# Performance work log

Measured on AMD Instinct MI355X. Metric: run time of the kernel, lower is better.

The kernel has to match this reference:

```python
import jax, jax.numpy as jnp
import numpy as np

N, E, F, H, L, G, O = 100000, 1600000, 128, 128, 4, 512, 10
BN_EPS = 1e-5


def setup_inputs() -> dict:
    key = jax.random.key(0)
    ks = jax.random.split(key, 12)
    x = jax.random.normal(ks[0], (N, F), dtype=jnp.float32)
    edge_index = jax.random.randint(ks[1], (2, E), 0, N, dtype=jnp.int32)
    batch = jnp.sort(jax.random.randint(ks[2], (N,), 0, G, dtype=jnp.int32))
    s = 1.0 / np.sqrt(H)
    # 4 GIN layers, input_dim == hidden_dim so params stack uniformly
    W1s = jax.random.uniform(ks[3], (L, F, H), jnp.float32, -s, s)
    b1s = jnp.zeros((L, H), jnp.float32)
    W2s = jax.random.uniform(ks[4], (L, H, H), jnp.float32, -s, s)
    b2s = jnp.zeros((L, H), jnp.float32)
    eps = jnp.zeros((L,), jnp.float32)  # learnable eps, init 0
    gammas = jnp.ones((L, H), jnp.float32)
    betas = jnp.zeros((L, H), jnp.float32)
    Din = F + L * H  # concatenated graph embedding dim
    so = 1.0 / np.sqrt(Din)
    Wout = jax.random.uniform(ks[5], (Din, O), jnp.float32, -so, so)
    bout = jnp.zeros((O,), jnp.float32)
    return {"x": x, "edge_index": edge_index, "batch": batch,
            "W1s": W1s, "b1s": b1s, "W2s": W2s, "b2s": b2s, "eps": eps,
            "gammas": gammas, "betas": betas, "Wout": Wout, "bout": bout}


def reference(x, edge_index, batch, W1s, b1s, W2s, b2s, eps, gammas, betas, Wout, bout):
    src, dst = edge_index[0], edge_index[1]
    n = x.shape[0]
    pooled = [jax.ops.segment_sum(x, batch, num_segments=G)]  # [G, F]
    h = x
    for l in range(W1s.shape[0]):
        # GINConv: MLP((1+eps)*h + sum_{j in N(i)} h_j)
        agg = jax.ops.segment_sum(h[src], dst, num_segments=n)  # [N, H]
        z = (1.0 + eps[l]) * h + agg
        z = jax.nn.relu(z @ W1s[l] + b1s[l]) @ W2s[l] + b2s[l]
        # BatchNorm1d (batch statistics, biased variance) + ReLU; dropout=identity (eval)
        mu = z.mean(axis=0)
        var = z.var(axis=0)
        z = (z - mu) * jax.lax.rsqrt(var + BN_EPS) * gammas[l] + betas[l]
        h = jax.nn.relu(z)
        pooled.append(jax.ops.segment_sum(h, batch, num_segments=G))  # [G, H]
    emb = jnp.concatenate(pooled, axis=1)  # [G, F + L*H]
    return emb @ Wout + bout  # [G, O]
```

## Files before the change

### kernel.cpp

```cpp
#include <hip/hip_runtime.h>
#include <hip/hip_bf16.h>

typedef __attribute__((ext_vector_type(8))) __bf16 bf16x8;
typedef __attribute__((ext_vector_type(4))) float f32x4;
typedef unsigned short u16;
typedef unsigned int u32;

constexpr int Nn = 100000;
constexpr int Ee = 1600000;
constexpr int Hd = 128;
constexpr int Ll = 4;
constexpr int Gg = 512;
constexpr int Oo = 10;
constexpr int Din = Hd + Ll * Hd;
constexpr int PSPLIT = 4;
constexpr int NBLK = (Nn + 127) / 128;
constexpr int AGG_BLKS = 8192;

constexpr int NB = 256;
constexpr int NPB = 392;
constexpr int BCAP = 8192;
constexpr int BATCH = 8192;
constexpr int NBATCH = (Ee + BATCH - 1) / BATCH;
constexpr int XCVT_BLKS = Nn * Hd / 8 / 256;
constexpr int WPREP_BLKS = Ll * 2 * Hd * Hd / 256;
constexpr float BN_EPS = 1e-5f;

__device__ __forceinline__ int swzb(int row, int bc) {
  return (row << 8) + (bc ^ ((row & 7) << 4));
}

__device__ __forceinline__ u16 f2bf(float f) {
  __hip_bfloat16 b = __float2bfloat16(f);
  u16 u;
  __builtin_memcpy(&u, &b, 2);
  return u;
}

__device__ __forceinline__ float bf2f(u32 u) { return __uint_as_float(u << 16); }

__device__ __forceinline__ int lower_bound_dev(const int* a, int n, int key) {
  int lo = 0, hi = n;
  while (lo < hi) { int mid = (lo + hi) >> 1; if (a[mid] < key) lo = mid + 1; else hi = mid; }
  return lo;
}

__device__ __forceinline__ void bn_param(const float* __restrict__ stats,
                                         const float* __restrict__ gammas,
                                         const float* __restrict__ betas,
                                         int prevL, int f, float& sc, float& sh) {
  const float invn = 1.0f / (float)Nn;
  float mu = stats[f] * invn;
  float var = stats[128 + f] * invn - mu * mu;
  sc = gammas[prevL * Hd + f] * rsqrtf(var + BN_EPS);
  sh = betas[prevL * Hd + f] - mu * sc;
}

__device__ __forceinline__ void gload_lds16(const void* g, void* l) {
  __builtin_amdgcn_global_load_lds((const __attribute__((address_space(1))) unsigned int*)g,
                                   (__attribute__((address_space(3))) unsigned int*)l, 16, 0, 0);
}

__global__ __launch_bounds__(256) void prep_kernel(const float* __restrict__ x, __hip_bfloat16* __restrict__ xb,
                                                   const float* __restrict__ W1s, const float* __restrict__ W2s,
                                                   __hip_bfloat16* __restrict__ wt,
                                                   int* __restrict__ gptr,
                                                   const int* __restrict__ batch, int* __restrict__ gb,
                                                   float* __restrict__ out, float* __restrict__ statsAll) {
  int b = blockIdx.x;
  int tid = threadIdx.x;
  if (b < XCVT_BLKS) {
    int i = b * 256 + tid;
    f32x4 v0 = *(const f32x4*)(x + (size_t)i * 8);
    f32x4 v1 = *(const f32x4*)(x + (size_t)i * 8 + 4);
    uint4 o;
    o.x = (u32)f2bf(v0[0]) | ((u32)f2bf(v0[1]) << 16);
    o.y = (u32)f2bf(v0[2]) | ((u32)f2bf(v0[3]) << 16);
    o.z = (u32)f2bf(v1[0]) | ((u32)f2bf(v1[1]) << 16);
    o.w = (u32)f2bf(v1[2]) | ((u32)f2bf(v1[3]) << 16);
    *(uint4*)((u16*)xb + (size_t)i * 8) = o;
  } else if (b < XCVT_BLKS + WPREP_BLKS) {
    int idx = (b - XCVT_BLKS) * 256 + tid;
    int l = idx >> 15;
    int w = (idx >> 14) & 1;
    int nn = (idx >> 7) & 127;
    int k = idx & 127;
    const float* W = w ? W2s : W1s;
    wt[idx] = __float2bfloat16(W[l * Hd * Hd + k * Hd + nn]);
  } else if (b == XCVT_BLKS + WPREP_BLKS) {
    gptr[tid] = tid * BCAP;
    for (int g = tid; g <= Gg; g += 256)
      gb[g] = (g == Gg) ? Nn : lower_bound_dev(batch, Nn, g);
  } else {
    for (int i = tid; i < Gg * Oo; i += 256) out[i] = 0.f;
    for (int i = tid; i < Ll * 256; i += 256) statsAll[i] = 0.f;
  }
}

__global__ __launch_bounds__(256) void binA_kernel(const int* __restrict__ src, const int* __restrict__ dst,
                                                   int* __restrict__ gptr, u32* __restrict__ buckets) {
  __shared__ int hist[NB];
  __shared__ int lbase[NB];
  __shared__ int lpos[NB];
  __shared__ int gbaseS[NB];
  __shared__ int scanT[NB];
  __shared__ u32 reorder[BATCH];
  const int tid = threadIdx.x;
  const int e0 = blockIdx.x * BATCH;
  const int n = min(BATCH, Ee - e0);

  hist[tid] = 0;
  __syncthreads();
  for (int k = tid; k < n; k += 256) {
    int d = dst[e0 + k];
    atomicAdd(&hist[d / NPB], 1);
  }
  __syncthreads();
  int v = hist[tid];
  scanT[tid] = v;
  __syncthreads();
  for (int off = 1; off < NB; off <<= 1) {
    int x = (tid >= off) ? scanT[tid - off] : 0;
    __syncthreads();
    scanT[tid] += x;
    __syncthreads();
  }
  lbase[tid] = scanT[tid] - v;
  lpos[tid] = 0;
  __syncthreads();
  for (int k = tid; k < n; k += 256) {
    int d = dst[e0 + k];
    int s = src[e0 + k];
    int b = d / NPB;
    int dlo = d - b * NPB;
    int p = lbase[b] + atomicAdd(&lpos[b], 1);
    reorder[p] = ((u32)dlo << 17) | (u32)s;
  }
  __syncthreads();
  if (hist[tid] > 0) gbaseS[tid] = atomicAdd(&gptr[tid], hist[tid]);
  __syncthreads();
  for (int p = tid; p < n; p += 256) {
    int lo = 0, hi = NB - 1;
    while (lo < hi) { int mid = (lo + hi + 1) >> 1; if (lbase[mid] <= p) lo = mid; else hi = mid - 1; }
    buckets[gbaseS[lo] + (p - lbase[lo])] = reorder[p];
  }
}

__global__ __launch_bounds__(512) void place_kernel(const u32* __restrict__ buckets,
                                                    const int* __restrict__ gptr,
                                                    int* __restrict__ indptr, int* __restrict__ adj) {
  __shared__ int cntS[NB];
  __shared__ int scanS[NB];
  __shared__ int ncnt[512];
  __shared__ int nofs[NPB];
  __shared__ int lcur[NPB];
  const int tid = threadIdx.x;
  const int b = blockIdx.x;

  if (tid < NB) {
    int c = gptr[tid] - tid * BCAP;
    cntS[tid] = c;
    scanS[tid] = c;
  }
  __syncthreads();
  for (int off = 1; off < NB; off <<= 1) {
    int x = 0;
    if (tid < NB && tid >= off) x = scanS[tid - off];
    __syncthreads();
    if (tid < NB) scanS[tid] += x;
    __syncthreads();
  }
  const int cnt = cntS[b];
  const int adjbase = scanS[b] - cnt;
  const int ebase = b * BCAP;
  const int node0 = b * NPB;
  const int nnodes = min(NPB, Nn - node0);

  ncnt[tid] = 0;
  if (tid < NPB) lcur[tid] = 0;
  __syncthreads();
  for (int k = tid; k < cnt; k += 512) atomicAdd(&ncnt[buckets[ebase + k] >> 17], 1);
  __syncthreads();
  int v = ncnt[tid];
  for (int off = 1; off < 512; off <<= 1) {
    int x = (tid >= off) ? ncnt[tid - off] : 0;
    __syncthreads();
    ncnt[tid] += x;
    __syncthreads();
  }
  if (tid < NPB) nofs[tid] = ncnt[tid] - v;
  __syncthreads();
  if (tid < nnodes) indptr[node0 + tid] = adjbase + nofs[tid];
  if (tid == 0 && b == 0) indptr[Nn] = Ee;
  for (int k = tid; k < cnt; k += 512) {
    u32 u = buckets[ebase + k];
    int dlo = u >> 17;
    int s = (int)(u & 0x1FFFFu);
    int p = atomicAdd(&lcur[dlo], 1);
    adj[adjbase + nofs[dlo] + p] = s;
  }
}

__global__ __launch_bounds__(256) void agg_kernel(const __hip_bfloat16* __restrict__ zprev,
                                                  const int* __restrict__ indptr,
                                                  const int* __restrict__ adj,
                                                  const float* __restrict__ stats,
                                                  const float* __restrict__ gammas,
                                                  const float* __restrict__ betas,
                                                  const float* __restrict__ epsp,
                                                  int layer, float negLim,
                                                  __hip_bfloat16* __restrict__ t) {
  const int gwave = blockIdx.x * 4 + (threadIdx.x >> 6);
  const int nwaves = AGG_BLKS * 4;
  const int lane = threadIdx.x & 63;
  const int cb = lane * 2;
  const u16* zp = (const u16*)zprev;
  float sc0 = 1.f, sh0 = 0.f, sc1 = 1.f, sh1 = 0.f;
  if (layer > 0) {
    bn_param(stats, gammas, betas, layer - 1, cb, sc0, sh0);
    bn_param(stats, gammas, betas, layer - 1, cb + 1, sc1, sh1);
  }
  const float eps1 = 1.0f + epsp[layer];

  for (int node = gwave; node < Nn; node += nwaves) {
    int s = __builtin_amdgcn_readfirstlane(indptr[node]);
    int e = __builtin_amdgcn_readfirstlane(indptr[node + 1]);
    float a0 = 0.f, a1 = 0.f;
    int p = s;
    while (p + 16 <= e) {
      u32 v[16];
      #pragma unroll
      for (int j = 0; j < 16; ++j) v[j] = *(const u32*)(zp + (size_t)adj[p + j] * Hd + cb);
      #pragma unroll
      for (int j = 0; j < 16; ++j) {
        a0 += fmaxf(fmaf(bf2f(v[j] & 0xffffu), sc0, sh0), negLim);
        a1 += fmaxf(fmaf(bf2f(v[j] >> 16), sc1, sh1), negLim);
      }
      p += 16;
    }
    if (p + 8 <= e) {
      u32 v[8];
      #pragma unroll
      for (int j = 0; j < 8; ++j) v[j] = *(const u32*)(zp + (size_t)adj[p + j] * Hd + cb);
      #pragma unroll
      for (int j = 0; j < 8; ++j) {
        a0 += fmaxf(fmaf(bf2f(v[j] & 0xffffu), sc0, sh0), negLim);
        a1 += fmaxf(fmaf(bf2f(v[j] >> 16), sc1, sh1), negLim);
      }
      p += 8;
    }
    if (p + 4 <= e) {
      u32 v[4];
      #pragma unroll
      for (int j = 0; j < 4; ++j) v[j] = *(const u32*)(zp + (size_t)adj[p + j] * Hd + cb);
      #pragma unroll
      for (int j = 0; j < 4; ++j) {
        a0 += fmaxf(fmaf(bf2f(v[j] & 0xffffu), sc0, sh0), negLim);
        a1 += fmaxf(fmaf(bf2f(v[j] >> 16), sc1, sh1), negLim);
      }
      p += 4;
    }
    for (; p < e; ++p) {
      u32 v0 = *(const u32*)(zp + (size_t)adj[p] * Hd + cb);
      a0 += fmaxf(fmaf(bf2f(v0 & 0xffffu), sc0, sh0), negLim);
      a1 += fmaxf(fmaf(bf2f(v0 >> 16), sc1, sh1), negLim);
    }
    u32 sv = *(const u32*)(zp + (size_t)node * Hd + cb);
    float s0 = fmaxf(fmaf(bf2f(sv & 0xffffu), sc0, sh0), negLim);
    float s1 = fmaxf(fmaf(bf2f(sv >> 16), sc1, sh1), negLim);
    float t0 = eps1 * s0 + a0;
    float t1 = eps1 * s1 + a1;
    *(u32*)((u16*)t + (size_t)node * Hd + cb) = (u32)f2bf(t0) | ((u32)f2bf(t1) << 16);
  }
}

__global__ __launch_bounds__(256) void mlp_kernel(const __hip_bfloat16* __restrict__ t,
                                                  const __hip_bfloat16* __restrict__ w1t,
                                                  const __hip_bfloat16* __restrict__ w2t,
                                                  const float* __restrict__ b1,
                                                  const float* __restrict__ b2,
                                                  __hip_bfloat16* __restrict__ z,
                                                  float* __restrict__ stats) {
  __shared__ __align__(16) unsigned char sA[32 * 1024];
  __shared__ __align__(16) unsigned char sW[32 * 1024];
  const int tid = threadIdx.x;
  const int m0 = blockIdx.x * 128;
  const int lane = tid & 63;
  const int wave = tid >> 6;

  #pragma unroll
  for (int blk = 0; blk < 8; ++blk) {
    const int chunk = wave * 512 + blk * 64 + lane;
    const int row = chunk >> 4, pos = chunk & 15;
    const int spos = pos ^ (row & 7);
    void* ldst = sA + (size_t)(wave * 512 + blk * 64) * 16;
    void* ldstW = sW + (size_t)(wave * 512 + blk * 64) * 16;
    gload_lds16((const unsigned char*)w1t + row * 256 + spos * 16, ldstW);
    gload_lds16((const unsigned char*)t + (size_t)(m0 + row) * 256 + spos * 16, ldst);
  }
  __syncthreads();

  const int lrow = lane & 15;
  const int lkb = (lane >> 4) << 4;
  const int wm = wave * 32;
  const int crow = (lane >> 4) << 2;

  f32x4 acc[2][8];
  #pragma unroll
  for (int a = 0; a < 2; ++a) {
    #pragma unroll
    for (int b = 0; b < 8; ++b) acc[a][b] = (f32x4){0.f, 0.f, 0.f, 0.f};
  }

  #pragma unroll
  for (int kk = 0; kk < 4; ++kk) {
    const int kb2 = kk * 64 + lkb;
    bf16x8 a0 = *(const bf16x8*)(sA + swzb(wm + lrow, kb2));
    bf16x8 a1 = *(const bf16x8*)(sA + swzb(wm + 16 + lrow, kb2));
    #pragma unroll
    for (int nf = 0; nf < 8; ++nf) {
      bf16x8 bfr = *(const bf16x8*)(sW + swzb(nf * 16 + lrow, kb2));
      acc[0][nf] = __builtin_amdgcn_mfma_f32_16x16x32_bf16(a0, bfr, acc[0][nf], 0, 0, 0);
      acc[1][nf] = __builtin_amdgcn_mfma_f32_16x16x32_bf16(a1, bfr, acc[1][nf], 0, 0, 0);
    }
  }
  __syncthreads();

  #pragma unroll
  for (int blk = 0; blk < 8; ++blk) {
    const int chunk = wave * 512 + blk * 64 + lane;
    const int row = chunk >> 4, pos = chunk & 15;
    const int spos = pos ^ (row & 7);
    gload_lds16((const unsigned char*)w2t + row * 256 + spos * 16,
                sW + (size_t)(wave * 512 + blk * 64) * 16);
  }
  #pragma unroll
  for (int nf = 0; nf < 8; ++nf) {
    const int col = nf * 16 + lrow;
    const float bb = b1[col];
    #pragma unroll
    for (int mf = 0; mf < 2; ++mf) {
      #pragma unroll
      for (int j = 0; j < 4; ++j) {
        float v = acc[mf][nf][j] + bb;
        v = v > 0.f ? v : 0.f;
        int row = wm + mf * 16 + crow + j;
        *(u16*)(sA + swzb(row, col * 2)) = f2bf(v);
      }
    }
  }
  __syncthreads();

  f32x4 acc2[2][8];
  #pragma unroll
  for (int a = 0; a < 2; ++a) {
    #pragma unroll
    for (int b = 0; b < 8; ++b) acc2[a][b] = (f32x4){0.f, 0.f, 0.f, 0.f};
  }
  #pragma unroll
  for (int kk = 0; kk < 4; ++kk) {
    const int kb2 = kk * 64 + lkb;
    bf16x8 a0 = *(const bf16x8*)(sA + swzb(wm + lrow, kb2));
    bf16x8 a1 = *(const bf16x8*)(sA + swzb(wm + 16 + lrow, kb2));
    #pragma unroll
    for (int nf = 0; nf < 8; ++nf) {
      bf16x8 bfr = *(const bf16x8*)(sW + swzb(nf * 16 + lrow, kb2));
      acc2[0][nf] = __builtin_amdgcn_mfma_f32_16x16x32_bf16(a0, bfr, acc2[0][nf], 0, 0, 0);
      acc2[1][nf] = __builtin_amdgcn_mfma_f32_16x16x32_bf16(a1, bfr, acc2[1][nf], 0, 0, 0);
    }
  }
  __syncthreads();

  float* sred = (float*)sA;
  float* qred = (float*)(sA + 2048);
  u16* zp = (u16*)z;
  #pragma unroll
  for (int nf = 0; nf < 8; ++nf) {
    const int col = nf * 16 + lrow;
    const float bb = b2[col];
    float s = 0.f, q = 0.f;
    #pragma unroll
    for (int mf = 0; mf < 2; ++mf) {
      #pragma unroll
      for (int j = 0; j < 4; ++j) {
        int grow = m0 + wm + mf * 16 + crow + j;
        if (grow < Nn) {
          float v = acc2[mf][nf][j] + bb;
          zp[(size_t)grow * Hd + col] = f2bf(v);
          s += v; q += v * v;
        }
      }
    }
    s += __shfl_xor(s, 16, 64); s += __shfl_xor(s, 32, 64);
    q += __shfl_xor(q, 16, 64); q += __shfl_xor(q, 32, 64);
    if (lane < 16) { sred[wave * 128 + col] = s; qred[wave * 128 + col] = q; }
  }
  __syncthreads();
  if (tid < 128) {
    float a = sred[tid] + sred[128 + tid] + sred[256 + tid] + sred[384 + tid];
    atomicAdd(&stats[tid], a);
  } else {
    int c = tid - 128;
    float a = qred[c] + qred[128 + c] + qred[256 + c] + qred[384 + c];
    atomicAdd(&stats[128 + c], a);
  }
}

__global__ __launch_bounds__(128) void pool_out_kernel(const __hip_bfloat16* __restrict__ xb,
                                                       const __hip_bfloat16* __restrict__ z0,
                                                       const __hip_bfloat16* __restrict__ z1,
                                                       const __hip_bfloat16* __restrict__ z2,
                                                       const __hip_bfloat16* __restrict__ z3,
                                                       const float* __restrict__ statsAll,
                                                       const float* __restrict__ gammas,
                                                       const float* __restrict__ betas,
                                                       const int* __restrict__ gb,
                                                       const float* __restrict__ Wout,
                                                       const float* __restrict__ bout,
                                                       float* __restrict__ out) {
  const int b = blockIdx.x;
  const int s = b / (Gg * PSPLIT);
  const int rem = b % (Gg * PSPLIT);
  const int g = rem / PSPLIT, sp = rem % PSPLIT;
  const __hip_bfloat16* zsrc = (s == 0) ? xb : (s == 1) ? z0 : (s == 2) ? z1 : (s == 3) ? z2 : z3;
  const float negLim = (s == 0) ? -3.4e38f : 0.f;
  const int colOff = s * Hd;
  const int c2 = (threadIdx.x & 63) * 2;
  const int rh = threadIdx.x >> 6;
  const int lane = threadIdx.x & 63;
  float sc0 = 1.f, sh0 = 0.f, sc1 = 1.f, sh1 = 0.f;
  if (s > 0) {
    bn_param(statsAll + (size_t)(s - 1) * 256, gammas, betas, s - 1, c2, sc0, sh0);
    bn_param(statsAll + (size_t)(s - 1) * 256, gammas, betas, s - 1, c2 + 1, sc1, sh1);
  }
  const int lo = gb[g], hi = gb[g + 1];
  const int len = hi - lo;
  const int chunk = (len + PSPLIT - 1) / PSPLIT;
  const int rs = lo + sp * chunk;
  const int re = min(rs + chunk, hi);
  const u16* zp = (const u16*)zsrc;
  float a0 = 0.f, a1 = 0.f, b0 = 0.f, b1v = 0.f, d0 = 0.f, d1 = 0.f, e0 = 0.f, e1 = 0.f;
  int i = rs + rh;
  for (; i + 6 < re; i += 8) {
    u32 v0 = *(const u32*)(zp + (size_t)i * Hd + c2);
    u32 v1 = *(const u32*)(zp + (size_t)(i + 2) * Hd + c2);
    u32 v2 = *(const u32*)(zp + (size_t)(i + 4) * Hd + c2);
    u32 v3 = *(const u32*)(zp + (size_t)(i + 6) * Hd + c2);
    a0 += fmaxf(fmaf(bf2f(v0 & 0xffffu), sc0, sh0), negLim);
    a1 += fmaxf(fmaf(bf2f(v0 >> 16), sc1, sh1), negLim);
    b0 += fmaxf(fmaf(bf2f(v1 & 0xffffu), sc0, sh0), negLim);
    b1v += fmaxf(fmaf(bf2f(v1 >> 16), sc1, sh1), negLim);
    d0 += fmaxf(fmaf(bf2f(v2 & 0xffffu), sc0, sh0), negLim);
    d1 += fmaxf(fmaf(bf2f(v2 >> 16), sc1, sh1), negLim);
    e0 += fmaxf(fmaf(bf2f(v3 & 0xffffu), sc0, sh0), negLim);
    e1 += fmaxf(fmaf(bf2f(v3 >> 16), sc1, sh1), negLim);
  }
  for (; i < re; i += 2) {
    u32 v = *(const u32*)(zp + (size_t)i * Hd + c2);
    a0 += fmaxf(fmaf(bf2f(v & 0xffffu), sc0, sh0), negLim);
    a1 += fmaxf(fmaf(bf2f(v >> 16), sc1, sh1), negLim);
  }
  a0 += b0 + d0 + e0;
  a1 += b1v + d1 + e1;

  float po[Oo];
  #pragma unroll
  for (int o = 0; o < Oo; ++o)
    po[o] = a0 * Wout[(colOff + c2) * Oo + o] + a1 * Wout[(colOff + c2 + 1) * Oo + o];
  #pragma unroll
  for (int off = 32; off > 0; off >>= 1) {
    #pragma unroll
    for (int o = 0; o < Oo; ++o) po[o] += __shfl_down(po[o], off, 64);
  }
  __shared__ float red[2][Oo];
  if (lane == 0) {
    #pragma unroll
    for (int o = 0; o < Oo; ++o) red[rh][o] = po[o];
  }
  __syncthreads();
  if (threadIdx.x < Oo) {
    float v = red[0][threadIdx.x] + red[1][threadIdx.x];
    if (s == 0 && sp == 0) v += bout[threadIdx.x];
    atomicAdd(&out[g * Oo + threadIdx.x], v);
  }
}

extern "C" void kernel_launch(void* const* d_in, const int* in_sizes, int n_in,
                              void* d_out, int out_size, void* d_ws, size_t ws_size,
                              hipStream_t stream) {
  (void)in_sizes; (void)n_in; (void)out_size;
  const float* x = (const float*)d_in[0];
  const int* ei = (const int*)d_in[1];
  const int* src = ei;
  const int* dst = ei + Ee;
  const int* batch = (const int*)d_in[2];
  const float* W1s = (const float*)d_in[3];
  const float* b1s = (const float*)d_in[4];
  const float* W2s = (const float*)d_in[5];
  const float* b2s = (const float*)d_in[6];
  const float* eps = (const float*)d_in[7];
  const float* gammas = (const float*)d_in[8];
  const float* betas = (const float*)d_in[9];
  const float* Wout = (const float*)d_in[10];
  const float* bout = (const float*)d_in[11];
  float* out = (float*)d_out;

  unsigned char* ws = (unsigned char*)d_ws;
  size_t off = 0;
  auto alloc = [&](size_t bytes) -> void* {
    void* p = ws + off;
    off = (off + bytes + 255) & ~size_t(255);
    return p;
  };
  __hip_bfloat16* xb = (__hip_bfloat16*)alloc((size_t)Nn * Hd * 2);
  __hip_bfloat16* z[Ll];
  for (int l = 0; l < Ll; ++l) z[l] = (__hip_bfloat16*)alloc((size_t)Nn * Hd * 2);
  __hip_bfloat16* t = (__hip_bfloat16*)alloc((size_t)Nn * Hd * 2);
  int* indptr = (int*)alloc((size_t)(Nn + 1) * 4);
  int* adj = (int*)alloc((size_t)Ee * 4);
  u32* buckets = (u32*)alloc((size_t)NB * BCAP * 4);
  int* gptr = (int*)alloc((size_t)NB * 4);
  int* gb = (int*)alloc((size_t)(Gg + 1) * 4);
  float* statsAll = (float*)alloc((size_t)Ll * 256 * 4);
  __hip_bfloat16* wt = (__hip_bfloat16*)alloc((size_t)Ll * 2 * Hd * Hd * 2);
  if (off > ws_size) return;

  prep_kernel<<<XCVT_BLKS + WPREP_BLKS + 2, 256, 0, stream>>>(x, xb, W1s, W2s, wt, gptr,
                                                              batch, gb, out, statsAll);

  binA_kernel<<<NBATCH, 256, 0, stream>>>(src, dst, gptr, buckets);
  place_kernel<<<NB, 512, 0, stream>>>(buckets, gptr, indptr, adj);

  const __hip_bfloat16* zprev = xb;
  for (int l = 0; l < Ll; ++l) {
    float negLim = (l == 0) ? -3.4e38f : 0.f;
    agg_kernel<<<AGG_BLKS, 256, 0, stream>>>(zprev, indptr, adj,
                                             statsAll + (size_t)(l > 0 ? l - 1 : 0) * 256,
                                             gammas, betas, eps, l, negLim, t);
    mlp_kernel<<<NBLK, 256, 0, stream>>>(
        t, wt + (size_t)l * 2 * Hd * Hd, wt + (size_t)l * 2 * Hd * Hd + Hd * Hd,
        b1s + l * Hd, b2s + l * Hd, z[l], statsAll + (size_t)l * 256);
    zprev = z[l];
  }

  pool_out_kernel<<<5 * Gg * PSPLIT, 128, 0, stream>>>(xb, z[0], z[1], z[2], z[3],
                                                       statsAll, gammas, betas, gb,
                                                       Wout, bout, out);
}
```

Baseline: 514.3 us.

## Process two nodes per wave in aggregation with 8-byte feature loads

Restructures the neighbor aggregation so each half-wave of 32 lanes handles one node, with each lane covering 4 features through 64-bit loads instead of 2 features through 32-bit loads. The goal is fewer, wider gather instructions and more nodes in flight per wave, which should improve memory-level parallelism in this latency-bound gather. In exchange, the two halves of a wave have different degrees and can diverge. The edge bounds are no longer scalar (readfirstlane is removed), and the main unroll drops from 16 to 8.

```diff
diff --git a/kernel.cpp b/kernel.cpp
--- a/kernel.cpp
+++ b/kernel.cpp
@@ -5,6 +5,7 @@
 typedef __attribute__((ext_vector_type(4))) float f32x4;
 typedef unsigned short u16;
 typedef unsigned int u32;
+typedef unsigned long long u64;
 
 constexpr int Nn = 100000;
 constexpr int Ee = 1600000;
@@ -213,64 +214,65 @@
   const int gwave = blockIdx.x * 4 + (threadIdx.x >> 6);
   const int nwaves = AGG_BLKS * 4;
   const int lane = threadIdx.x & 63;
-  const int cb = lane * 2;
+  const int half = lane >> 5;
+  const int fb = (lane & 31) * 4;
   const u16* zp = (const u16*)zprev;
-  float sc0 = 1.f, sh0 = 0.f, sc1 = 1.f, sh1 = 0.f;
+  float sc[4] = {1.f, 1.f, 1.f, 1.f}, sh[4] = {0.f, 0.f, 0.f, 0.f};
   if (layer > 0) {
-    bn_param(stats, gammas, betas, layer - 1, cb, sc0, sh0);
-    bn_param(stats, gammas, betas, layer - 1, cb + 1, sc1, sh1);
+    #pragma unroll
+    for (int i = 0; i < 4; ++i) bn_param(stats, gammas, betas, layer - 1, fb + i, sc[i], sh[i]);
   }
   const float eps1 = 1.0f + epsp[layer];
 
-  for (int node = gwave; node < Nn; node += nwaves) {
-    int s = __builtin_amdgcn_readfirstlane(indptr[node]);
-    int e = __builtin_amdgcn_readfirstlane(indptr[node + 1]);
-    float a0 = 0.f, a1 = 0.f;
-    int p = s;
-    while (p + 16 <= e) {
-      u32 v[16];
+  for (int pair = gwave; pair * 2 < Nn; pair += nwaves) {
+    const int node = pair * 2 + half;
+    int p = indptr[node];
+    const int e = indptr[node + 1];
+    float a0 = 0.f, a1 = 0.f, a2 = 0.f, a3 = 0.f;
+    while (p + 8 <= e) {
+      u64 v[8];
       #pragma unroll
-      for (int j = 0; j < 16; ++j) v[j] = *(const u32*)(zp + (size_t)adj[p + j] * Hd + cb);
-      #pragma unroll
-      for (int j = 0; j < 16; ++j) {
-        a0 += fmaxf(fmaf(bf2f(v[j] & 0xffffu), sc0, sh0), negLim);
-        a1 += fmaxf(fmaf(bf2f(v[j] >> 16), sc1, sh1), negLim);
-      }
-      p += 16;
-    }
-    if (p + 8 <= e) {
-      u32 v[8];
-      #pragma unroll
-      for (int j = 0; j < 8; ++j) v[j] = *(const u32*)(zp + (size_t)adj[p + j] * Hd + cb);
+      for (int j = 0; j < 8; ++j) v[j] = *(const u64*)(zp + (size_t)adj[p + j] * Hd + fb);
       #pragma unroll
       for (int j = 0; j < 8; ++j) {
-        a0 += fmaxf(fmaf(bf2f(v[j] & 0xffffu), sc0, sh0), negLim);
-        a1 += fmaxf(fmaf(bf2f(v[j] >> 16), sc1, sh1), negLim);
+        a0 += fmaxf(fmaf(bf2f((u32)(v[j] & 0xffffu)), sc[0], sh[0]), negLim);
+        a1 += fmaxf(fmaf(bf2f((u32)((v[j] >> 16) & 0xffffu)), sc[1], sh[1]), negLim);
+        a2 += fmaxf(fmaf(bf2f((u32)((v[j] >> 32) & 0xffffu)), sc[2], sh[2]), negLim);
+        a3 += fmaxf(fmaf(bf2f((u32)(v[j] >> 48)), sc[3], sh[3]), negLim);
       }
       p += 8;
     }
     if (p + 4 <= e) {
-      u32 v[4];
+      u64 v[4];
       #pragma unroll
-      for (int j = 0; j < 4; ++j) v[j] = *(const u32*)(zp + (size_t)adj[p + j] * Hd + cb);
+      for (int j = 0; j < 4; ++j) v[j] = *(const u64*)(zp + (size_t)adj[p + j] * Hd + fb);
       #pragma unroll
       for (int j = 0; j < 4; ++j) {
-        a0 += fmaxf(fmaf(bf2f(v[j] & 0xffffu), sc0, sh0), negLim);
-        a1 += fmaxf(fmaf(bf2f(v[j] >> 16), sc1, sh1), negLim);
+        a0 += fmaxf(fmaf(bf2f((u32)(v[j] & 0xffffu)), sc[0], sh[0]), negLim);
+        a1 += fmaxf(fmaf(bf2f((u32)((v[j] >> 16) & 0xffffu)), sc[1], sh[1]), negLim);
+        a2 += fmaxf(fmaf(bf2f((u32)((v[j] >> 32) & 0xffffu)), sc[2], sh[2]), negLim);
+        a3 += fmaxf(fmaf(bf2f((u32)(v[j] >> 48)), sc[3], sh[3]), negLim);
       }
       p += 4;
     }
     for (; p < e; ++p) {
-      u32 v0 = *(const u32*)(zp + (size_t)adj[p] * Hd + cb);
-      a0 += fmaxf(fmaf(bf2f(v0 & 0xffffu), sc0, sh0), negLim);
-      a1 += fmaxf(fmaf(bf2f(v0 >> 16), sc1, sh1), negLim);
-    }
-    u32 sv = *(const u32*)(zp + (size_t)node * Hd + cb);
-    float s0 = fmaxf(fmaf(bf2f(sv & 0xffffu), sc0, sh0), negLim);
-    float s1 = fmaxf(fmaf(bf2f(sv >> 16), sc1, sh1), negLim);
+      u64 v = *(const u64*)(zp + (size_t)adj[p] * Hd + fb);
+      a0 += fmaxf(fmaf(bf2f((u32)(v & 0xffffu)), sc[0], sh[0]), negLim);
+      a1 += fmaxf(fmaf(bf2f((u32)((v >> 16) & 0xffffu)), sc[1], sh[1]), negLim);
+      a2 += fmaxf(fmaf(bf2f((u32)((v >> 32) & 0xffffu)), sc[2], sh[2]), negLim);
+      a3 += fmaxf(fmaf(bf2f((u32)(v >> 48)), sc[3], sh[3]), negLim);
+    }
+    u64 sv = *(const u64*)(zp + (size_t)node * Hd + fb);
+    float s0 = fmaxf(fmaf(bf2f((u32)(sv & 0xffffu)), sc[0], sh[0]), negLim);
+    float s1 = fmaxf(fmaf(bf2f((u32)((sv >> 16) & 0xffffu)), sc[1], sh[1]), negLim);
+    float s2 = fmaxf(fmaf(bf2f((u32)((sv >> 32) & 0xffffu)), sc[2], sh[2]), negLim);
+    float s3 = fmaxf(fmaf(bf2f((u32)(sv >> 48)), sc[3], sh[3]), negLim);
     float t0 = eps1 * s0 + a0;
     float t1 = eps1 * s1 + a1;
-    *(u32*)((u16*)t + (size_t)node * Hd + cb) = (u32)f2bf(t0) | ((u32)f2bf(t1) << 16);
+    float t2 = eps1 * s2 + a2;
+    float t3 = eps1 * s3 + a3;
+    u64 o = (u64)f2bf(t0) | ((u64)f2bf(t1) << 16) | ((u64)f2bf(t2) << 32) | ((u64)f2bf(t3) << 48);
+    *(u64*)((u16*)t + (size_t)node * Hd + fb) = o;
   }
 }
 
```

New measurement: 526.0 us. 2.3% more time.
